# Kernel optimization log

Measured on AMD Instinct MI355X. Metric: run time of the kernel, lower is better.

## Reference

```python
import jax, jax.numpy as jnp
import numpy as np

EPS = 1e-12


def setup_inputs() -> dict:
    key = jax.random.key(0)
    k1, k2 = jax.random.split(key)
    batch, seq_len, hidden, conv_size = 64, 4096, 128, 16
    input_tensor = jax.random.normal(k1, (batch, seq_len, hidden), dtype=jnp.float32)
    conv_weight = jax.random.normal(k2, (1, conv_size, hidden), dtype=jnp.float32) * 0.02
    ln_weight = jnp.ones((hidden,), dtype=jnp.float32)
    ln_bias = jnp.zeros((hidden,), dtype=jnp.float32)
    return {"input_tensor": input_tensor, "conv_weight": conv_weight,
            "ln_weight": ln_weight, "ln_bias": ln_bias}


def reference(input_tensor, conv_weight, ln_weight, ln_bias):
    # input_tensor: [B, S, H]; conv_weight: [1, K, H] zero-padded to length S
    seq_len = input_tensor.shape[1]
    x = jnp.fft.rfft(input_tensor, axis=1, norm="ortho")  # [B, S//2+1, H] complex
    pad = seq_len - conv_weight.shape[1]
    w = jnp.pad(conv_weight, ((0, 0), (0, pad), (0, 0)))
    w = jnp.fft.rfft(w, axis=1, norm="ortho")  # [1, S//2+1, H]
    y = jnp.fft.irfft(x * w, n=seq_len, axis=1, norm="ortho")  # [B, S, H]
    # dropout is identity at inference; residual + TF-style LayerNorm
    h = y + input_tensor
    u = h.mean(-1, keepdims=True)
    s = ((h - u) ** 2).mean(-1, keepdims=True)
    return ln_weight * (h - u) / jnp.sqrt(s + EPS) + ln_bias
```

## Files before the change

### kernel.cpp

```cpp
#include <hip/hip_runtime.h>


constexpr int S = 4096;
constexpr int H = 128;
constexpr int K = 16;
constexpr int CHUNK = 64;
constexpr int GROUP = 16;

__global__ __launch_bounds__(256)
void fconv_ln_kernel(const float* __restrict__ x,
                     const float* __restrict__ wconv,
                     const float* __restrict__ lnw,
                     const float* __restrict__ lnb,
                     float* __restrict__ out)
{
    const int wid  = (blockIdx.x * blockDim.x + threadIdx.x) >> 6;
    const int lane = threadIdx.x & 63;

    const int chunksPerSeq = S / CHUNK;
    const int b  = wid / chunksPerSeq;
    const int t0 = (wid % chunksPerSeq) * CHUNK;

    const int c2 = lane * 2;

    float2 w[K];
#pragma unroll
    for (int k = 0; k < K; ++k)
        w[k] = *reinterpret_cast<const float2*>(&wconv[k * H + c2]);

    const float2 gamma = *reinterpret_cast<const float2*>(&lnw[c2]);
    const float2 beta  = *reinterpret_cast<const float2*>(&lnb[c2]);

    const float* xb = x   + (size_t)b * S * H;
    float*       ob = out + (size_t)b * S * H;

    float2 ring[2 * GROUP];

#pragma unroll
    for (int s = 0; s < GROUP; ++s) {
        int t = (t0 - GROUP + s + S) & (S - 1);
        ring[s] = *reinterpret_cast<const float2*>(&xb[(size_t)t * H + c2]);
    }

    for (int tb = 0; tb < CHUNK; tb += GROUP) {
#pragma unroll
        for (int j = 0; j < GROUP; ++j) {
            ring[GROUP + j] = *reinterpret_cast<const float2*>(
                &xb[(size_t)(t0 + tb + j) * H + c2]);
        }

#pragma unroll
        for (int j = 0; j < GROUP; ++j) {
            float ax = 0.f, ay = 0.f;
#pragma unroll
            for (int k = 0; k < K; ++k) {
                const float2 v = ring[GROUP + j - k];
                ax = fmaf(w[k].x, v.x, ax);
                ay = fmaf(w[k].y, v.y, ay);
            }
            const float2 xt = ring[GROUP + j];
            float hx = fmaf(ax, 0.015625f, xt.x);
            float hy = fmaf(ay, 0.015625f, xt.y);

            float s1 = hx + hy;
            float s2 = hx * hx + hy * hy;
#pragma unroll
            for (int m = 1; m < 64; m <<= 1) {
                s1 += __shfl_xor(s1, m, 64);
                s2 += __shfl_xor(s2, m, 64);
            }
            const float u   = s1 * (1.0f / H);
            const float var = fmaf(s2, 1.0f / H, -u * u);
            const float inv = rsqrtf(var + 1e-12f);

            float2 o;
            o.x = fmaf(gamma.x * inv, hx - u, beta.x);
            o.y = fmaf(gamma.y * inv, hy - u, beta.y);
            *reinterpret_cast<float2*>(&ob[(size_t)(t0 + tb + j) * H + c2]) = o;
        }

#pragma unroll
        for (int j = 0; j < GROUP; ++j)
            ring[j] = ring[GROUP + j];
    }
}

extern "C" void kernel_launch(void* const* d_in, const int* in_sizes, int n_in,
                              void* d_out, int out_size, void* d_ws, size_t ws_size,
                              hipStream_t stream)
{
    const float* x     = (const float*)d_in[0];
    const float* wconv = (const float*)d_in[1];
    const float* lnw   = (const float*)d_in[2];
    const float* lnb   = (const float*)d_in[3];
    float*       out   = (float*)d_out;

    const int Bsz = in_sizes[0] / (S * H);
    const int totalWaves = Bsz * (S / CHUNK);
    const int threads = 256;
    const int blocks  = totalWaves * 64 / threads;

    hipLaunchKernelGGL(fconv_ln_kernel, dim3(blocks), dim3(threads), 0, stream,
                       x, wconv, lnw, lnb, out);
}
```

Before: 259.8 us.

## Prefetch next row group and use DPP wave reductions for LayerNorm stats

Restructures the per-wave loop so the next group of 8 rows is loaded into registers while the current group is computed, software-pipelining global loads against the conv and LayerNorm math. It also replaces the shuffle-based butterfly reduction with DPP row operations plus a readlane for the mean and variance sums, cutting cross-lane instruction cost. The history buffer becomes separate hist/cur/nxt arrays, which may raise register pressure and change occupancy.

```diff
diff --git a/kernel.cpp b/kernel.cpp
--- a/kernel.cpp
+++ b/kernel.cpp
@@ -5,7 +5,23 @@
 constexpr int H = 128;
 constexpr int K = 16;
 constexpr int CHUNK = 64;
-constexpr int GROUP = 16;
+constexpr int G = 8;
+
+template <int CTRL, int ROWMASK>
+__device__ __forceinline__ float dpp_add(float x) {
+    int y = __builtin_amdgcn_update_dpp(0, __float_as_int(x), CTRL, ROWMASK, 0xf, true);
+    return x + __int_as_float(y);
+}
+
+__device__ __forceinline__ float wave_sum(float x) {
+    x = dpp_add<0x111, 0xf>(x);
+    x = dpp_add<0x112, 0xf>(x);
+    x = dpp_add<0x114, 0xf>(x);
+    x = dpp_add<0x118, 0xf>(x);
+    x = dpp_add<0x142, 0xa>(x);
+    x = dpp_add<0x143, 0xc>(x);
+    return __int_as_float(__builtin_amdgcn_readlane(__float_as_int(x), 63));
+}
 
 __global__ __launch_bounds__(256)
 void fconv_ln_kernel(const float* __restrict__ x,
@@ -34,41 +50,42 @@
     const float* xb = x   + (size_t)b * S * H;
     float*       ob = out + (size_t)b * S * H;
 
-    float2 ring[2 * GROUP];
+    float2 hist[K];
+    float2 cur[G];
+    float2 nxt[G];
 
 #pragma unroll
-    for (int s = 0; s < GROUP; ++s) {
-        int t = (t0 - GROUP + s + S) & (S - 1);
-        ring[s] = *reinterpret_cast<const float2*>(&xb[(size_t)t * H + c2]);
+    for (int s = 0; s < K; ++s) {
+        int t = (t0 - K + s + S) & (S - 1);
+        hist[s] = *reinterpret_cast<const float2*>(&xb[(size_t)t * H + c2]);
     }
+#pragma unroll
+    for (int j = 0; j < G; ++j)
+        cur[j] = *reinterpret_cast<const float2*>(&xb[(size_t)(t0 + j) * H + c2]);
 
-    for (int tb = 0; tb < CHUNK; tb += GROUP) {
+    for (int tb = 0; tb < CHUNK; tb += G) {
+        if (tb + G < CHUNK) {
 #pragma unroll
-        for (int j = 0; j < GROUP; ++j) {
-            ring[GROUP + j] = *reinterpret_cast<const float2*>(
-                &xb[(size_t)(t0 + tb + j) * H + c2]);
+            for (int j = 0; j < G; ++j)
+                nxt[j] = *reinterpret_cast<const float2*>(
+                    &xb[(size_t)(t0 + tb + G + j) * H + c2]);
         }
 
 #pragma unroll
-        for (int j = 0; j < GROUP; ++j) {
+        for (int j = 0; j < G; ++j) {
             float ax = 0.f, ay = 0.f;
 #pragma unroll
             for (int k = 0; k < K; ++k) {
-                const float2 v = ring[GROUP + j - k];
+                const float2 v = (k <= j) ? cur[j - k] : hist[K + j - k];
                 ax = fmaf(w[k].x, v.x, ax);
                 ay = fmaf(w[k].y, v.y, ay);
             }
-            const float2 xt = ring[GROUP + j];
+            const float2 xt = cur[j];
             float hx = fmaf(ax, 0.015625f, xt.x);
             float hy = fmaf(ay, 0.015625f, xt.y);
 
-            float s1 = hx + hy;
-            float s2 = hx * hx + hy * hy;
-#pragma unroll
-            for (int m = 1; m < 64; m <<= 1) {
-                s1 += __shfl_xor(s1, m, 64);
-                s2 += __shfl_xor(s2, m, 64);
-            }
+            const float s1 = wave_sum(hx + hy);
+            const float s2 = wave_sum(hx * hx + hy * hy);
             const float u   = s1 * (1.0f / H);
             const float var = fmaf(s2, 1.0f / H, -u * u);
             const float inv = rsqrtf(var + 1e-12f);
@@ -80,8 +97,11 @@
         }
 
 #pragma unroll
-        for (int j = 0; j < GROUP; ++j)
-            ring[j] = ring[GROUP + j];
+        for (int s = 0; s < K - G; ++s) hist[s] = hist[s + G];
+#pragma unroll
+        for (int j = 0; j < G; ++j)     hist[K - G + j] = cur[j];
+#pragma unroll
+        for (int j = 0; j < G; ++j)     cur[j] = nxt[j];
     }
 }
 
```

Result: faster. 243.0 us (-6.5%).
